# Optimization experiments

Measured on AMD Instinct MI355X. Metric: run time of the kernel, lower is better.

## Reference

```python
import jax, jax.numpy as jnp
import numpy as np

D_MODEL = 1024
NUM_HEADS = 16
D_K = D_MODEL // NUM_HEADS
B, S = 4, 2048


def setup_inputs() -> dict:
    key = jax.random.key(0)
    ks = jax.random.split(key, 7)
    scale = 1.0 / np.sqrt(D_MODEL)
    return {
        "q": jax.random.normal(ks[0], (B, S, D_MODEL), jnp.float32),
        "k": jax.random.normal(ks[1], (B, S, D_MODEL), jnp.float32),
        "v": jax.random.normal(ks[2], (B, S, D_MODEL), jnp.float32),
        "w_q": jax.random.normal(ks[3], (D_MODEL, D_MODEL), jnp.float32) * scale,
        "w_k": jax.random.normal(ks[4], (D_MODEL, D_MODEL), jnp.float32) * scale,
        "w_v": jax.random.normal(ks[5], (D_MODEL, D_MODEL), jnp.float32) * scale,
        "w_o": jax.random.normal(ks[6], (D_MODEL, D_MODEL), jnp.float32) * scale,
    }


def reference(q, k, v, w_q, w_k, w_v, w_o):
    # projections: [B,S,D] @ [D,D]
    qh = (q @ w_q).reshape(B, -1, NUM_HEADS, D_K).transpose(0, 2, 1, 3)  # [B,H,S,dk]
    kh = (k @ w_k).reshape(B, -1, NUM_HEADS, D_K).transpose(0, 2, 1, 3)
    vh = (v @ w_v).reshape(B, -1, NUM_HEADS, D_K).transpose(0, 2, 1, 3)
    scores = jnp.einsum("bhqd,bhkd->bhqk", qh, kh) / jnp.sqrt(jnp.float32(D_K))
    attn = jax.nn.softmax(scores, axis=-1)  # dropout is identity in eval mode
    out = jnp.einsum("bhqk,bhkd->bhqd", attn, vh)  # [B,H,S,dk]
    out = out.transpose(0, 2, 1, 3).reshape(B, -1, D_MODEL)
    return out @ w_o, attn
```

## Files before the change

kernel.cpp:

```cpp
#include <hip/hip_runtime.h>


typedef __attribute__((ext_vector_type(8))) short bf16x8;
typedef __attribute__((ext_vector_type(4))) float f32x4;
typedef __attribute__((ext_vector_type(8))) unsigned short u16x8;
typedef __attribute__((ext_vector_type(4))) unsigned short u16x4;

#define L2E 1.4426950408889634f

__device__ __forceinline__ unsigned short f2bf(float x) {
    unsigned u = __float_as_uint(x);
    u += 0x7FFFu + ((u >> 16) & 1u);
    return (unsigned short)(u >> 16);
}

__device__ __forceinline__ uint2 pk4(f32x4 v) {
    unsigned r0, r1;
    asm("v_cvt_pk_bf16_f32 %0, %1, %2" : "=v"(r0) : "v"(v[0]), "v"(v[1]));
    asm("v_cvt_pk_bf16_f32 %0, %1, %2" : "=v"(r1) : "v"(v[2]), "v"(v[3]));
    return make_uint2(r0, r1);
}

__device__ __forceinline__ void gll16(const void* g, void* l) {
    __builtin_amdgcn_global_load_lds(
        (const __attribute__((address_space(1))) void*)g,
        (__attribute__((address_space(3))) void*)l, 16, 0, 0);
}

__global__ __launch_bounds__(256) void cvt3(
    const float* __restrict__ q, const float* __restrict__ k, const float* __restrict__ v,
    unsigned short* __restrict__ qb, unsigned short* __restrict__ kb, unsigned short* __restrict__ vb)
{
    int b = blockIdx.x;
    int which = b >> 12;
    const float* src = which == 0 ? q : (which == 1 ? k : v);
    unsigned short* dst = which == 0 ? qb : (which == 1 ? kb : vb);
    size_t off = ((size_t)(b & 4095) * 256 + threadIdx.x) * 8;
    float4 x0 = *(const float4*)(src + off);
    float4 x1 = *(const float4*)(src + off + 4);
    u16x8 o;
    o[0] = f2bf(x0.x); o[1] = f2bf(x0.y); o[2] = f2bf(x0.z); o[3] = f2bf(x0.w);
    o[4] = f2bf(x1.x); o[5] = f2bf(x1.y); o[6] = f2bf(x1.z); o[7] = f2bf(x1.w);
    *(u16x8*)(dst + off) = o;
}

__global__ __launch_bounds__(256) void wtrans(
    const float* __restrict__ w0, const float* __restrict__ w1,
    const float* __restrict__ w2, const float* __restrict__ w3,
    unsigned short* __restrict__ o0, unsigned short* __restrict__ o1,
    unsigned short* __restrict__ o2, unsigned short* __restrict__ o3)
{
    __shared__ float T[64 * 68];
    int b = blockIdx.x;
    int wi = b >> 8, tile = b & 255;
    int k0 = (tile >> 4) * 64, n0 = (tile & 15) * 64;
    const float* W = wi == 0 ? w0 : (wi == 1 ? w1 : (wi == 2 ? w2 : w3));
    unsigned short* O = wi == 0 ? o0 : (wi == 1 ? o1 : (wi == 2 ? o2 : o3));
    float scale = (wi == 0) ? 0.125f : 1.0f;
    int t = threadIdx.x;
#pragma unroll
    for (int i = 0; i < 4; i++) {
        int idx = i * 256 + t;
        int r = idx >> 4, ch = idx & 15;
        float4 vv = *(const float4*)(W + (size_t)(k0 + r) * 1024 + n0 + ch * 4);
        *(float4*)(&T[r * 68 + ch * 4]) = vv;
    }
    __syncthreads();
#pragma unroll
    for (int i = 0; i < 2; i++) {
        int idx = i * 256 + t;
        int n = idx >> 3, ch = idx & 7;
        u16x8 o;
#pragma unroll
        for (int jj = 0; jj < 8; jj++) o[jj] = f2bf(T[(ch * 8 + jj) * 68 + n] * scale);
        *(u16x8*)(O + (size_t)(n0 + n) * 1024 + k0 + ch * 8) = o;
    }
}

template<int MODE>
__global__ __launch_bounds__(256) void gemm128(
    const unsigned short* __restrict__ A0, const unsigned short* __restrict__ A1, const unsigned short* __restrict__ A2,
    const unsigned short* __restrict__ B0, const unsigned short* __restrict__ B1, const unsigned short* __restrict__ B2,
    void* O0, void* O1, void* O2)
{
    constexpr int K = 1024, NK = 32;
    __shared__ unsigned short As[2][128 * 32];
    __shared__ unsigned short Bs[2][128 * 32];
    const int t = threadIdx.x, lane = t & 63, w = t >> 6;
    const int z = blockIdx.z;
    const unsigned short* A  = z == 0 ? A0 : (z == 1 ? A1 : A2);
    const unsigned short* Bt = z == 0 ? B0 : (z == 1 ? B1 : B2);
    void* O = z == 0 ? O0 : (z == 1 ? O1 : O2);
    const bool vt = (MODE == 0) && (z == 2);
    int bid = blockIdx.x;
    int xcd = bid & 7, seq = bid >> 3;
    int npan = seq >> 3, mpan = ((seq & 7) << 3) + xcd;
    int m0 = mpan * 128, n0 = npan * 128;
    int wr = w >> 1, wc = w & 1;
    int qhi = lane >> 4, rr = lane & 15;

    auto stage = [&](int buf, int kt) {
#pragma unroll
        for (int i = 0; i < 2; i++) {
            int o = ((w * 2 + i) << 10) + (lane << 4);
            int r = o >> 6, c = o & 63;
            int sc = c ^ (((r >> 1) & 3) << 4);
            gll16((const char*)A + ((size_t)(m0 + r) * K + kt * 32) * 2 + sc,
                  (char*)&As[buf][0] + ((w * 2 + i) << 10));
        }
#pragma unroll
        for (int i = 0; i < 2; i++) {
            int o = ((w * 2 + i) << 10) + (lane << 4);
            int r = o >> 6, c = o & 63;
            int sc = c ^ (((r >> 1) & 3) << 4);
            gll16((const char*)Bt + ((size_t)(n0 + r) * K + kt * 32) * 2 + sc,
                  (char*)&Bs[buf][0] + ((w * 2 + i) << 10));
        }
    };

    f32x4 acc[4][4] = {};
    stage(0, 0);
    __syncthreads();
    int buf = 0;
    for (int kt = 0; kt < NK; kt++) {
        if (kt + 1 < NK) stage(buf ^ 1, kt + 1);
        const char* as = (const char*)&As[buf][0];
        const char* bs = (const char*)&Bs[buf][0];
        bf16x8 a[4], b[4];
#pragma unroll
        for (int mi = 0; mi < 4; mi++) {
            int r = wr * 64 + mi * 16 + rr;
            a[mi] = *(const bf16x8*)(as + r * 64 + ((qhi << 4) ^ (((r >> 1) & 3) << 4)));
        }
#pragma unroll
        for (int ni = 0; ni < 4; ni++) {
            int r = wc * 64 + ni * 16 + rr;
            b[ni] = *(const bf16x8*)(bs + r * 64 + ((qhi << 4) ^ (((r >> 1) & 3) << 4)));
        }
        if (vt) {
#pragma unroll
            for (int mi = 0; mi < 4; mi++)
#pragma unroll
                for (int ni = 0; ni < 4; ni++)
                    acc[mi][ni] = __builtin_amdgcn_mfma_f32_16x16x32_bf16(a[mi], b[ni], acc[mi][ni], 0, 0, 0);
        } else {
#pragma unroll
            for (int mi = 0; mi < 4; mi++)
#pragma unroll
                for (int ni = 0; ni < 4; ni++)
                    acc[mi][ni] = __builtin_amdgcn_mfma_f32_16x16x32_bf16(b[ni], a[mi], acc[mi][ni], 0, 0, 0);
        }
        __syncthreads();
        buf ^= 1;
    }

    if (MODE == 1) {
#pragma unroll
        for (int mi = 0; mi < 4; mi++) {
            int m = m0 + wr * 64 + mi * 16 + rr;
#pragma unroll
            for (int ni = 0; ni < 4; ni++) {
                int n = n0 + wc * 64 + ni * 16 + qhi * 4;
                f32x4 o = acc[mi][ni];
                __builtin_nontemporal_store(o, (f32x4*)((float*)O + (size_t)m * 1024 + n));
            }
        }
    } else if (vt) {
        unsigned short* Vt = (unsigned short*)O;
#pragma unroll
        for (int mi = 0; mi < 4; mi++) {
            int m = m0 + wr * 64 + mi * 16 + qhi * 4;
#pragma unroll
            for (int ni = 0; ni < 4; ni++) {
                int n = n0 + wc * 64 + ni * 16 + rr;
                int bh = (m >> 11) * 16 + (n >> 6);
                *(uint2*)(Vt + ((size_t)bh * 64 + (n & 63)) * 2048 + (m & 2047)) = pk4(acc[mi][ni]);
            }
        }
    } else {
        unsigned short* Oh = (unsigned short*)O;
#pragma unroll
        for (int mi = 0; mi < 4; mi++) {
            int m = m0 + wr * 64 + mi * 16 + rr;
#pragma unroll
            for (int ni = 0; ni < 4; ni++) {
                int n = n0 + wc * 64 + ni * 16 + qhi * 4;
                size_t idx = (((size_t)((m >> 11) * 16 + (n >> 6))) * 2048 + (m & 2047)) * 64 + (n & 63);
                *(uint2*)(Oh + idx) = pk4(acc[mi][ni]);
            }
        }
    }
}

__global__ __launch_bounds__(256) void attn64(
    const unsigned short* __restrict__ Qh, const unsigned short* __restrict__ Kh,
    const unsigned short* __restrict__ Vt, float* __restrict__ attn,
    unsigned short* __restrict__ ctx)
{
    __shared__ unsigned short Ks[2][64 * 64];
    __shared__ unsigned short Vs[2][64 * 64];
    __shared__ unsigned short Ps[4][16 * 72];
    const int t = threadIdx.x, lane = t & 63, w = t >> 6;
    int bid = blockIdx.x;
    int rm = (bid & 7) * 256 + (bid >> 3);
    int bh = rm >> 5, rb = rm & 31;
    int qhi = lane >> 4, rr = lane & 15;
    int q0 = rb * 64 + w * 16;

    const unsigned short* qb = Qh + ((size_t)bh * 2048 + q0 + rr) * 64;
    bf16x8 aq0 = *(const bf16x8*)(qb + qhi * 8);
    bf16x8 aq1 = *(const bf16x8*)(qb + 32 + qhi * 8);

    auto stageK = [&](int buf, int ct) {
#pragma unroll
        for (int i = 0; i < 2; i++) {
            int o = ((w * 2 + i) << 10) + (lane << 4);
            int r = o >> 7, c = o & 127;
            int sc = c ^ ((r & 7) << 4);
            gll16((const char*)Kh + (size_t)(bh * 2048 + ct * 64 + r) * 128 + sc,
                  (char*)&Ks[buf][0] + ((w * 2 + i) << 10));
        }
    };
    auto stageV = [&](int buf, int ct) {
#pragma unroll
        for (int i = 0; i < 2; i++) {
            int o = ((w * 2 + i) << 10) + (lane << 4);
            int r = o >> 7, c = o & 127;
            int sc = c ^ ((r & 7) << 4);
            gll16((const char*)Vt + (size_t)(bh * 64 + r) * 4096 + ct * 128 + sc,
                  (char*)&Vs[buf][0] + ((w * 2 + i) << 10));
        }
    };

    f32x4 sv = {0.f, 0.f, 0.f, 0.f};
    stageK(0, 0);
    __syncthreads();
    int buf = 0;
    for (int ct = 0; ct < 32; ct++) {
        if (ct < 31) stageK(buf ^ 1, ct + 1);
        const char* ks = (const char*)&Ks[buf][0];
#pragma unroll
        for (int n = 0; n < 4; n++) {
            int r = n * 16 + rr;
            int sw = (r & 7) << 4;
            bf16x8 b0 = *(const bf16x8*)(ks + r * 128 + ((qhi << 4) ^ sw));
            bf16x8 b1 = *(const bf16x8*)(ks + r * 128 + ((64 | (qhi << 4)) ^ sw));
            f32x4 z4 = {0.f, 0.f, 0.f, 0.f};
            f32x4 s = __builtin_amdgcn_mfma_f32_16x16x32_bf16(b0, aq0, z4, 0, 0, 0);
            s = __builtin_amdgcn_mfma_f32_16x16x32_bf16(b1, aq1, s, 0, 0, 0);
#pragma unroll
            for (int j = 0; j < 4; j++) sv[j] += exp2f(s[j] * L2E);
        }
        __syncthreads();
        buf ^= 1;
    }
    float lsum = sv[0] + sv[1] + sv[2] + sv[3];
    lsum += __shfl_xor(lsum, 16);
    lsum += __shfl_xor(lsum, 32);
    float lr2 = -__log2f(lsum);

    stageK(0, 0); stageV(0, 0);
    __syncthreads();
    buf = 0;
    float* awr = attn + (size_t)bh * 2048 * 2048 + (size_t)(q0 + rr) * 2048;
    f32x4 acco[4] = {};
    for (int ct = 0; ct < 32; ct++) {
        if (ct < 31) { stageK(buf ^ 1, ct + 1); stageV(buf ^ 1, ct + 1); }
        const char* ks = (const char*)&Ks[buf][0];
        f32x4 s[4];
#pragma unroll
        for (int n = 0; n < 4; n++) {
            int r = n * 16 + rr;
            int sw = (r & 7) << 4;
            bf16x8 b0 = *(const bf16x8*)(ks + r * 128 + ((qhi << 4) ^ sw));
            bf16x8 b1 = *(const bf16x8*)(ks + r * 128 + ((64 | (qhi << 4)) ^ sw));
            f32x4 z4 = {0.f, 0.f, 0.f, 0.f};
            s[n] = __builtin_amdgcn_mfma_f32_16x16x32_bf16(b0, aq0, z4, 0, 0, 0);
            s[n] = __builtin_amdgcn_mfma_f32_16x16x32_bf16(b1, aq1, s[n], 0, 0, 0);
        }
#pragma unroll
        for (int n = 0; n < 4; n++) {
            f32x4 pv;
#pragma unroll
            for (int j = 0; j < 4; j++) pv[j] = exp2f(s[n][j] * L2E + lr2);
            __builtin_nontemporal_store(pv, (f32x4*)(awr + ct * 64 + n * 16 + qhi * 4));
            *(uint2*)((char*)&Ps[w][0] + rr * 144 + n * 32 + qhi * 8) = pk4(pv);
        }
        bf16x8 pa0 = *(const bf16x8*)((const char*)&Ps[w][0] + rr * 144 + (qhi << 4));
        bf16x8 pa1 = *(const bf16x8*)((const char*)&Ps[w][0] + rr * 144 + 64 + (qhi << 4));
        const char* vs = (const char*)&Vs[buf][0];
#pragma unroll
        for (int nd = 0; nd < 4; nd++) {
            int r = nd * 16 + rr;
            int sw = (r & 7) << 4;
            bf16x8 v0 = *(const bf16x8*)(vs + r * 128 + ((qhi << 4) ^ sw));
            bf16x8 v1 = *(const bf16x8*)(vs + r * 128 + ((64 | (qhi << 4)) ^ sw));
            acco[nd] = __builtin_amdgcn_mfma_f32_16x16x32_bf16(pa0, v0, acco[nd], 0, 0, 0);
            acco[nd] = __builtin_amdgcn_mfma_f32_16x16x32_bf16(pa1, v1, acco[nd], 0, 0, 0);
        }
        __syncthreads();
        buf ^= 1;
    }
    int b_ = bh >> 4, h_ = bh & 15;
#pragma unroll
    for (int nd = 0; nd < 4; nd++)
#pragma unroll
        for (int j = 0; j < 4; j++) {
            int qr = q0 + qhi * 4 + j;
            int d = nd * 16 + rr;
            ctx[((size_t)b_ * 2048 + qr) * 1024 + h_ * 64 + d] = f2bf(acco[nd][j]);
        }
}

extern "C" void kernel_launch(void* const* d_in, const int* in_sizes, int n_in,
                              void* d_out, int out_size, void* d_ws, size_t ws_size,
                              hipStream_t stream)
{
    (void)in_sizes; (void)n_in; (void)out_size; (void)ws_size;
    const float* q  = (const float*)d_in[0];
    const float* k  = (const float*)d_in[1];
    const float* v  = (const float*)d_in[2];
    const float* wq = (const float*)d_in[3];
    const float* wk = (const float*)d_in[4];
    const float* wv = (const float*)d_in[5];
    const float* wo = (const float*)d_in[6];
    char* ws = (char*)d_ws;
    const size_t M1 = 1ull << 20;
    unsigned short* qbf = (unsigned short*)(ws);
    unsigned short* kbf = (unsigned short*)(ws + 16 * M1);
    unsigned short* vbf = (unsigned short*)(ws + 32 * M1);
    unsigned short* wqt = (unsigned short*)(ws + 48 * M1);
    unsigned short* wkt = (unsigned short*)(ws + 50 * M1);
    unsigned short* wvt = (unsigned short*)(ws + 52 * M1);
    unsigned short* wot = (unsigned short*)(ws + 54 * M1);
    unsigned short* Qh  = (unsigned short*)(ws + 56 * M1);
    unsigned short* Kh  = (unsigned short*)(ws + 72 * M1);
    unsigned short* Vt  = (unsigned short*)(ws + 88 * M1);
    unsigned short* ctx = kbf;
    float* out0 = (float*)d_out;
    float* attn = out0 + (size_t)8192 * 1024;

    cvt3<<<12288, 256, 0, stream>>>(q, k, v, qbf, kbf, vbf);
    wtrans<<<1024, 256, 0, stream>>>(wq, wk, wv, wo, wqt, wkt, wvt, wot);
    gemm128<0><<<dim3(512, 1, 3), 256, 0, stream>>>(qbf, kbf, vbf, wqt, wkt, wvt,
                                                    (void*)Qh, (void*)Kh, (void*)Vt);
    attn64<<<2048, 256, 0, stream>>>(Qh, Kh, Vt, attn, ctx);
    gemm128<1><<<dim3(512, 1, 1), 256, 0, stream>>>(ctx, ctx, ctx, wot, wot, wot,
                                                    (void*)out0, (void*)out0, (void*)out0);
}
```

Measured before the change: 447.0 us.

## Rework attention kernel to 32x32 MFMA with 128-row query tiles

Attention now uses 32x32x16 bf16 MFMA tiles, with each wave handling 32 query rows and each block 128 rows, which halves the grid and halves how often K/V tiles are staged per query. The P matrix is kept in registers and fed straight into the PV MFMA by packing the accumulator layout, so the per-wave LDS round trip for P is gone. Context stores become vectorised 8-byte writes. Attention-probability stores switch from nontemporal to ordinary stores, and register pressure goes up, which may reduce occupancy.

```diff
diff --git a/kernel.cpp b/kernel.cpp
--- a/kernel.cpp
+++ b/kernel.cpp
@@ -3,8 +3,10 @@
 
 typedef __attribute__((ext_vector_type(8))) short bf16x8;
 typedef __attribute__((ext_vector_type(4))) float f32x4;
+typedef __attribute__((ext_vector_type(16))) float f32x16;
 typedef __attribute__((ext_vector_type(8))) unsigned short u16x8;
 typedef __attribute__((ext_vector_type(4))) unsigned short u16x4;
+typedef __attribute__((ext_vector_type(4))) unsigned int u32x4;
 
 #define L2E 1.4426950408889634f
 
@@ -192,24 +194,25 @@
     }
 }
 
-__global__ __launch_bounds__(256) void attn64(
+__global__ __launch_bounds__(256) void attn128(
     const unsigned short* __restrict__ Qh, const unsigned short* __restrict__ Kh,
     const unsigned short* __restrict__ Vt, float* __restrict__ attn,
     unsigned short* __restrict__ ctx)
 {
     __shared__ unsigned short Ks[2][64 * 64];
     __shared__ unsigned short Vs[2][64 * 64];
-    __shared__ unsigned short Ps[4][16 * 72];
     const int t = threadIdx.x, lane = t & 63, w = t >> 6;
     int bid = blockIdx.x;
-    int rm = (bid & 7) * 256 + (bid >> 3);
-    int bh = rm >> 5, rb = rm & 31;
-    int qhi = lane >> 4, rr = lane & 15;
-    int q0 = rb * 64 + w * 16;
-
-    const unsigned short* qb = Qh + ((size_t)bh * 2048 + q0 + rr) * 64;
-    bf16x8 aq0 = *(const bf16x8*)(qb + qhi * 8);
-    bf16x8 aq1 = *(const bf16x8*)(qb + 32 + qhi * 8);
+    int rm = (bid & 7) * 128 + (bid >> 3);
+    int bh = rm >> 4, rb = rm & 15;
+    int hl = lane >> 5;
+    int cq = lane & 31;
+    int q0 = rb * 128 + w * 32;
+
+    const unsigned short* qb = Qh + ((size_t)bh * 2048 + q0 + cq) * 64;
+    bf16x8 bq[4];
+#pragma unroll
+    for (int ks = 0; ks < 4; ks++) bq[ks] = *(const bf16x8*)(qb + ks * 16 + hl * 8);
 
     auto stageK = [&](int buf, int ct) {
 #pragma unroll
@@ -232,83 +235,90 @@
         }
     };
 
-    f32x4 sv = {0.f, 0.f, 0.f, 0.f};
+    float su = 0.f;
     stageK(0, 0);
     __syncthreads();
     int buf = 0;
     for (int ct = 0; ct < 32; ct++) {
         if (ct < 31) stageK(buf ^ 1, ct + 1);
-        const char* ks = (const char*)&Ks[buf][0];
-#pragma unroll
-        for (int n = 0; n < 4; n++) {
-            int r = n * 16 + rr;
-            int sw = (r & 7) << 4;
-            bf16x8 b0 = *(const bf16x8*)(ks + r * 128 + ((qhi << 4) ^ sw));
-            bf16x8 b1 = *(const bf16x8*)(ks + r * 128 + ((64 | (qhi << 4)) ^ sw));
-            f32x4 z4 = {0.f, 0.f, 0.f, 0.f};
-            f32x4 s = __builtin_amdgcn_mfma_f32_16x16x32_bf16(b0, aq0, z4, 0, 0, 0);
-            s = __builtin_amdgcn_mfma_f32_16x16x32_bf16(b1, aq1, s, 0, 0, 0);
-#pragma unroll
-            for (int j = 0; j < 4; j++) sv[j] += exp2f(s[j] * L2E);
+        const char* ksL = (const char*)&Ks[buf][0];
+#pragma unroll
+        for (int kcT = 0; kcT < 2; kcT++) {
+            f32x16 s = {};
+#pragma unroll
+            for (int ks = 0; ks < 4; ks++) {
+                int r = kcT * 32 + cq;
+                int c = (ks * 32 + hl * 16) ^ ((r & 7) << 4);
+                bf16x8 kf = *(const bf16x8*)(ksL + r * 128 + c);
+                s = __builtin_amdgcn_mfma_f32_32x32x16_bf16(kf, bq[ks], s, 0, 0, 0);
+            }
+#pragma unroll
+            for (int j = 0; j < 16; j++) su += exp2f(s[j] * L2E);
         }
         __syncthreads();
         buf ^= 1;
     }
-    float lsum = sv[0] + sv[1] + sv[2] + sv[3];
-    lsum += __shfl_xor(lsum, 16);
-    lsum += __shfl_xor(lsum, 32);
-    float lr2 = -__log2f(lsum);
+    su += __shfl_xor(su, 32);
+    float lr2 = -__log2f(su);
 
     stageK(0, 0); stageV(0, 0);
     __syncthreads();
     buf = 0;
-    float* awr = attn + (size_t)bh * 2048 * 2048 + (size_t)(q0 + rr) * 2048;
-    f32x4 acco[4] = {};
+    float* awr = attn + (size_t)bh * 2048 * 2048 + (size_t)(q0 + cq) * 2048;
+    f32x16 acco[2] = {};
     for (int ct = 0; ct < 32; ct++) {
         if (ct < 31) { stageK(buf ^ 1, ct + 1); stageV(buf ^ 1, ct + 1); }
-        const char* ks = (const char*)&Ks[buf][0];
-        f32x4 s[4];
-#pragma unroll
-        for (int n = 0; n < 4; n++) {
-            int r = n * 16 + rr;
-            int sw = (r & 7) << 4;
-            bf16x8 b0 = *(const bf16x8*)(ks + r * 128 + ((qhi << 4) ^ sw));
-            bf16x8 b1 = *(const bf16x8*)(ks + r * 128 + ((64 | (qhi << 4)) ^ sw));
-            f32x4 z4 = {0.f, 0.f, 0.f, 0.f};
-            s[n] = __builtin_amdgcn_mfma_f32_16x16x32_bf16(b0, aq0, z4, 0, 0, 0);
-            s[n] = __builtin_amdgcn_mfma_f32_16x16x32_bf16(b1, aq1, s[n], 0, 0, 0);
-        }
-#pragma unroll
-        for (int n = 0; n < 4; n++) {
-            f32x4 pv;
-#pragma unroll
-            for (int j = 0; j < 4; j++) pv[j] = exp2f(s[n][j] * L2E + lr2);
-            __builtin_nontemporal_store(pv, (f32x4*)(awr + ct * 64 + n * 16 + qhi * 4));
-            *(uint2*)((char*)&Ps[w][0] + rr * 144 + n * 32 + qhi * 8) = pk4(pv);
-        }
-        bf16x8 pa0 = *(const bf16x8*)((const char*)&Ps[w][0] + rr * 144 + (qhi << 4));
-        bf16x8 pa1 = *(const bf16x8*)((const char*)&Ps[w][0] + rr * 144 + 64 + (qhi << 4));
-        const char* vs = (const char*)&Vs[buf][0];
-#pragma unroll
-        for (int nd = 0; nd < 4; nd++) {
-            int r = nd * 16 + rr;
-            int sw = (r & 7) << 4;
-            bf16x8 v0 = *(const bf16x8*)(vs + r * 128 + ((qhi << 4) ^ sw));
-            bf16x8 v1 = *(const bf16x8*)(vs + r * 128 + ((64 | (qhi << 4)) ^ sw));
-            acco[nd] = __builtin_amdgcn_mfma_f32_16x16x32_bf16(pa0, v0, acco[nd], 0, 0, 0);
-            acco[nd] = __builtin_amdgcn_mfma_f32_16x16x32_bf16(pa1, v1, acco[nd], 0, 0, 0);
+        const char* ksL = (const char*)&Ks[buf][0];
+        const char* vsL = (const char*)&Vs[buf][0];
+#pragma unroll
+        for (int kcT = 0; kcT < 2; kcT++) {
+            f32x16 s = {};
+#pragma unroll
+            for (int ks = 0; ks < 4; ks++) {
+                int r = kcT * 32 + cq;
+                int c = (ks * 32 + hl * 16) ^ ((r & 7) << 4);
+                bf16x8 kf = *(const bf16x8*)(ksL + r * 128 + c);
+                s = __builtin_amdgcn_mfma_f32_32x32x16_bf16(kf, bq[ks], s, 0, 0, 0);
+            }
+            unsigned wAv[4], wBv[4];
+#pragma unroll
+            for (int g = 0; g < 4; g++) {
+                f32x4 pv;
+#pragma unroll
+                for (int j = 0; j < 4; j++) pv[j] = exp2f(s[g * 4 + j] * L2E + lr2);
+                *(f32x4*)(awr + ct * 64 + kcT * 32 + g * 8 + hl * 4) = pv;
+                asm("v_cvt_pk_bf16_f32 %0, %1, %2" : "=v"(wAv[g]) : "v"(pv[0]), "v"(pv[1]));
+                asm("v_cvt_pk_bf16_f32 %0, %1, %2" : "=v"(wBv[g]) : "v"(pv[2]), "v"(pv[3]));
+            }
+#pragma unroll
+            for (int ksl = 0; ksl < 2; ksl++) {
+                int ksp = kcT * 2 + ksl;
+                u32x4 fw = {wAv[2 * ksl], wBv[2 * ksl], wAv[2 * ksl + 1], wBv[2 * ksl + 1]};
+                bf16x8 pf = *(bf16x8*)&fw;
+#pragma unroll
+                for (int dT = 0; dT < 2; dT++) {
+                    int r = dT * 32 + cq;
+                    int sw = (r & 7) << 4;
+                    uint2 lo8 = *(const uint2*)(vsL + r * 128 + ((ksp * 32 + hl * 8) ^ sw));
+                    uint2 hi8 = *(const uint2*)(vsL + r * 128 + ((ksp * 32 + 16 + hl * 8) ^ sw));
+                    u32x4 vw = {lo8.x, lo8.y, hi8.x, hi8.y};
+                    bf16x8 vf = *(bf16x8*)&vw;
+                    acco[dT] = __builtin_amdgcn_mfma_f32_32x32x16_bf16(vf, pf, acco[dT], 0, 0, 0);
+                }
+            }
         }
         __syncthreads();
         buf ^= 1;
     }
     int b_ = bh >> 4, h_ = bh & 15;
-#pragma unroll
-    for (int nd = 0; nd < 4; nd++)
-#pragma unroll
-        for (int j = 0; j < 4; j++) {
-            int qr = q0 + qhi * 4 + j;
-            int d = nd * 16 + rr;
-            ctx[((size_t)b_ * 2048 + qr) * 1024 + h_ * 64 + d] = f2bf(acco[nd][j]);
+    unsigned short* cw = ctx + ((size_t)b_ * 2048 + q0 + cq) * 1024 + h_ * 64;
+#pragma unroll
+    for (int dT = 0; dT < 2; dT++)
+#pragma unroll
+        for (int g = 0; g < 4; g++) {
+            f32x4 cv = {acco[dT][4 * g], acco[dT][4 * g + 1],
+                        acco[dT][4 * g + 2], acco[dT][4 * g + 3]};
+            *(uint2*)(cw + dT * 32 + g * 8 + hl * 4) = pk4(cv);
         }
 }
 
@@ -344,7 +354,7 @@
     wtrans<<<1024, 256, 0, stream>>>(wq, wk, wv, wo, wqt, wkt, wvt, wot);
     gemm128<0><<<dim3(512, 1, 3), 256, 0, stream>>>(qbf, kbf, vbf, wqt, wkt, wvt,
                                                     (void*)Qh, (void*)Kh, (void*)Vt);
-    attn64<<<2048, 256, 0, stream>>>(Qh, Kh, Vt, attn, ctx);
+    attn128<<<1024, 256, 0, stream>>>(Qh, Kh, Vt, attn, ctx);
     gemm128<1><<<dim3(512, 1, 1), 256, 0, stream>>>(ctx, ctx, ctx, wot, wot, wot,
                                                     (void*)out0, (void*)out0, (void*)out0);
 }
```

After: 619.2 us. 1.39x slower.

## Keep softmax probabilities in registers for PV MFMA, dropping LDS round-trip

Applied to the files above, without the earlier changes.

The attention kernel no longer writes the bf16 probability tile to per-wave shared memory and reads it back. It packs the probabilities in registers and swaps the MFMA operand order, so the S-accumulator layout feeds the PV product directly, reading V with matching 8-byte fragments. It also makes the context output store vectorized per row instead of scalar bf16 stores. The LDS traffic and wait on the P tile go away, at the cost of twice as many narrower V LDS reads.

```diff
diff --git a/kernel.cpp b/kernel.cpp
--- a/kernel.cpp
+++ b/kernel.cpp
@@ -4,7 +4,7 @@
 typedef __attribute__((ext_vector_type(8))) short bf16x8;
 typedef __attribute__((ext_vector_type(4))) float f32x4;
 typedef __attribute__((ext_vector_type(8))) unsigned short u16x8;
-typedef __attribute__((ext_vector_type(4))) unsigned short u16x4;
+typedef __attribute__((ext_vector_type(4))) unsigned int u32x4;
 
 #define L2E 1.4426950408889634f
 
@@ -199,7 +199,6 @@
 {
     __shared__ unsigned short Ks[2][64 * 64];
     __shared__ unsigned short Vs[2][64 * 64];
-    __shared__ unsigned short Ps[4][16 * 72];
     const int t = threadIdx.x, lane = t & 63, w = t >> 6;
     int bid = blockIdx.x;
     int rm = (bid & 7) * 256 + (bid >> 3);
@@ -278,38 +277,40 @@
             s[n] = __builtin_amdgcn_mfma_f32_16x16x32_bf16(b0, aq0, z4, 0, 0, 0);
             s[n] = __builtin_amdgcn_mfma_f32_16x16x32_bf16(b1, aq1, s[n], 0, 0, 0);
         }
+        unsigned wA[4], wB[4];
 #pragma unroll
         for (int n = 0; n < 4; n++) {
             f32x4 pv;
 #pragma unroll
             for (int j = 0; j < 4; j++) pv[j] = exp2f(s[n][j] * L2E + lr2);
             __builtin_nontemporal_store(pv, (f32x4*)(awr + ct * 64 + n * 16 + qhi * 4));
-            *(uint2*)((char*)&Ps[w][0] + rr * 144 + n * 32 + qhi * 8) = pk4(pv);
-        }
-        bf16x8 pa0 = *(const bf16x8*)((const char*)&Ps[w][0] + rr * 144 + (qhi << 4));
-        bf16x8 pa1 = *(const bf16x8*)((const char*)&Ps[w][0] + rr * 144 + 64 + (qhi << 4));
+            asm("v_cvt_pk_bf16_f32 %0, %1, %2" : "=v"(wA[n]) : "v"(pv[0]), "v"(pv[1]));
+            asm("v_cvt_pk_bf16_f32 %0, %1, %2" : "=v"(wB[n]) : "v"(pv[2]), "v"(pv[3]));
+        }
         const char* vs = (const char*)&Vs[buf][0];
 #pragma unroll
-        for (int nd = 0; nd < 4; nd++) {
-            int r = nd * 16 + rr;
-            int sw = (r & 7) << 4;
-            bf16x8 v0 = *(const bf16x8*)(vs + r * 128 + ((qhi << 4) ^ sw));
-            bf16x8 v1 = *(const bf16x8*)(vs + r * 128 + ((64 | (qhi << 4)) ^ sw));
-            acco[nd] = __builtin_amdgcn_mfma_f32_16x16x32_bf16(pa0, v0, acco[nd], 0, 0, 0);
-            acco[nd] = __builtin_amdgcn_mfma_f32_16x16x32_bf16(pa1, v1, acco[nd], 0, 0, 0);
+        for (int kb = 0; kb < 2; kb++) {
+            u32x4 fw = {wA[2 * kb], wB[2 * kb], wA[2 * kb + 1], wB[2 * kb + 1]};
+            bf16x8 pf = *(bf16x8*)&fw;
+#pragma unroll
+            for (int db = 0; db < 4; db++) {
+                int r = db * 16 + rr;
+                int sw = (r & 7) << 4;
+                uint2 lo8 = *(const uint2*)(vs + r * 128 + ((kb * 64 + qhi * 8) ^ sw));
+                uint2 hi8 = *(const uint2*)(vs + r * 128 + ((kb * 64 + 32 + qhi * 8) ^ sw));
+                u32x4 vw = {lo8.x, lo8.y, hi8.x, hi8.y};
+                bf16x8 vf = *(bf16x8*)&vw;
+                acco[db] = __builtin_amdgcn_mfma_f32_16x16x32_bf16(vf, pf, acco[db], 0, 0, 0);
+            }
         }
         __syncthreads();
         buf ^= 1;
     }
     int b_ = bh >> 4, h_ = bh & 15;
-#pragma unroll
-    for (int nd = 0; nd < 4; nd++)
-#pragma unroll
-        for (int j = 0; j < 4; j++) {
-            int qr = q0 + qhi * 4 + j;
-            int d = nd * 16 + rr;
-            ctx[((size_t)b_ * 2048 + qr) * 1024 + h_ * 64 + d] = f2bf(acco[nd][j]);
-        }
+    unsigned short* cw = ctx + ((size_t)b_ * 2048 + q0 + rr) * 1024 + h_ * 64;
+#pragma unroll
+    for (int db = 0; db < 4; db++)
+        *(uint2*)(cw + db * 16 + qhi * 4) = pk4(acco[db]);
 }
 
 extern "C" void kernel_launch(void* const* d_in, const int* in_sizes, int n_in,
```

After: 459.4 us. 2.8% more time.
